# Optimization experiments

Hardware: AMD Instinct MI355X
Metric: run time of the kernel (lower is better)

## Reference

```python
import jax, jax.numpy as jnp
import numpy as np
from jax import lax

NUM_MASKS = 100
NUM_CLASSES = 81  # 80 + 1
KERNEL_DIM = 256
BIAS_PRIOR = float(-np.log((1 - 0.01) / 0.01))


def setup_inputs() -> dict:
    key = jax.random.key(0)
    ks = jax.random.split(key, 12)
    B, C, H, W = 4, 256, 160, 160
    D = C  # expand_dim = in_channels * num_groups
    inp = {
        "features": jax.random.normal(ks[0], (B, C, H, W), jnp.float32),
        # iam_conv: Conv2d(C, num_masks, 3, padding=1)
        "w_iam": jax.random.normal(ks[1], (NUM_MASKS, C, 3, 3), jnp.float32) * 0.01,
        "b_iam": jnp.full((NUM_MASKS,), BIAS_PRIOR, jnp.float32),
        "softmax_bias": jnp.ones((1,), jnp.float32),
        # fc: Linear(D, D), xavier-ish
        "w_fc": jax.random.normal(ks[2], (D, D), jnp.float32) * (1.0 / np.sqrt(D)),
        "b_fc": jnp.zeros((D,), jnp.float32),
        "w_cls": jax.random.normal(ks[3], (NUM_CLASSES, D), jnp.float32) * 0.01,
        "b_cls": jnp.full((NUM_CLASSES,), BIAS_PRIOR, jnp.float32),
        "w_ker": jax.random.normal(ks[4], (KERNEL_DIM, D), jnp.float32) * 0.01,
        "b_ker": jnp.zeros((KERNEL_DIM,), jnp.float32),
        "w_obj": jax.random.normal(ks[5], (1, D), jnp.float32) * (1.0 / np.sqrt(D)),
        "b_obj": jnp.zeros((1,), jnp.float32),
        "w_box": jax.random.normal(ks[6], (4, D), jnp.float32) * 0.01,
        "b_box": jnp.zeros((4,), jnp.float32),
    }
    return inp


def reference(features, w_iam, b_iam, softmax_bias, w_fc, b_fc,
              w_cls, b_cls, w_ker, b_ker, w_obj, b_obj, w_box, b_box):
    B, C, H, W = features.shape
    # conv score map: (B, num_masks, H, W)
    iam = lax.conv_general_dilated(
        features, w_iam, window_strides=(1, 1), padding="SAME",
        dimension_numbers=("NCHW", "OIHW", "NCHW")) + b_iam[None, :, None, None]
    # num_groups == 1: single group iam
    iam_flat = iam.reshape(B, NUM_MASKS, H * W)
    # softmax over HW with learned scalar bias (bias shifts uniformly -> no-op math-wise but kept faithful)
    iam_prob = jax.nn.softmax(iam_flat + softmax_bias[0], axis=-1)  # (B, M, HW)
    # spatial attention pooling: bmm(prob, feats^T) -> (B, M, C)
    inst = jnp.einsum("bmp,bcp->bmc", iam_prob, features.reshape(B, C, H * W))
    # prev_inst_features is None -> skip fc_fuse
    inst = jax.nn.relu(inst @ w_fc.T + b_fc)
    pred_logits = inst @ w_cls.T + b_cls
    pred_kernel = inst @ w_ker.T + b_ker
    pred_scores = inst @ w_obj.T + b_obj
    pred_bboxes = inst @ w_box.T + b_box
    return (pred_logits, pred_kernel, pred_scores, pred_bboxes, iam, inst)
```

## Files before the change

kernel.cpp:

```cpp
#include <hip/hip_runtime.h>
#include <hip/hip_bf16.h>

typedef __attribute__((ext_vector_type(8))) short bf16x8;
typedef __attribute__((ext_vector_type(4))) float f32x4;

#define HW_ 25600
#define HP_ 162
#define WP_ 162

__device__ __forceinline__ unsigned short f2bf(float f) {
    union { float f; unsigned u; } x; x.f = f;
    unsigned r = x.u + 0x7FFFu + ((x.u >> 16) & 1u);
    return (unsigned short)(r >> 16);
}

typedef const __attribute__((address_space(1))) unsigned int* gas_t;
typedef __attribute__((address_space(3))) unsigned int* las_t;
__device__ __forceinline__ void gl_lds16(const void* g, void* l) {
    __builtin_amdgcn_global_load_lds((gas_t)g, (las_t)l, 16, 0, 0);
}

__global__ __launch_bounds__(256) void k_prep(const float* __restrict__ w_iam,
                                              unsigned short* __restrict__ wp,
                                              unsigned short* __restrict__ fpad) {
    int bid = blockIdx.x;
    if (bid < 1152) {
        int idx = bid * 256 + threadIdx.x;
        int stage = idx >> 12;
        int r = idx & 4095;
        int m = r >> 5, cl = r & 31;
        int tap = stage >> 3, kc = stage & 7;
        int jj = (cl >> 3) ^ ((m >> 1) & 3);
        int c = kc * 32 + jj * 8 + (cl & 7);
        int dy = (tap * 11) >> 5, dx = tap - dy * 3;
        float v = (m < 100) ? w_iam[((m * 256 + c) * 3 + dy) * 3 + dx] : 0.f;
        wp[idx] = f2bf(v);
    } else {
        int idx = (bid - 1152) * 256 + threadIdx.x;
        const int perb = 164864;
        if (idx >= 4 * perb) return;
        int b = idx / perb;
        int r = idx - b * perb;
        int hp, wpp, c;
        if (r < 82944) {
            hp = (r < 41472) ? 0 : 161;
            int r2 = r % 41472;
            wpp = r2 >> 8; c = r2 & 255;
        } else {
            r -= 82944;
            wpp = (r < 40960) ? 0 : 161;
            int r2 = r % 40960;
            hp = 1 + (r2 >> 8); c = r2 & 255;
        }
        fpad[((b * HP_ + hp) * WP_ + wpp) * 256 + c] = 0;
    }
}

__global__ __launch_bounds__(256) void k_convert(const float* __restrict__ feat,
                                                 unsigned short* __restrict__ fpad) {
    int bid = blockIdx.x;
    int b = bid / 640;
    int h = (bid >> 2) % 160;
    int c0 = (bid & 3) * 64;
    __shared__ float tile[64][161];
    int t = threadIdx.x;
    const float4* src4 = (const float4*)(feat + ((long)(b * 256 + c0) * 160 + h) * 160);
    #pragma unroll
    for (int s = 0; s < 10; ++s) {
        int q = t + s * 256;
        int ci = q / 40;
        int w4 = q - ci * 40;
        float4 v = src4[(long)ci * 6400 + w4];
        tile[ci][w4 * 4 + 0] = v.x;
        tile[ci][w4 * 4 + 1] = v.y;
        tile[ci][w4 * 4 + 2] = v.z;
        tile[ci][w4 * 4 + 3] = v.w;
    }
    __syncthreads();
    int co = (t & 7) * 8, wq = t >> 3;
    unsigned short* dst = fpad + ((long)(b * HP_ + h + 1) * WP_ + 1) * 256 + c0 + co;
    #pragma unroll
    for (int wp = 0; wp < 5; ++wp) {
        int w = wq + wp * 32;
        bf16x8 v;
        #pragma unroll
        for (int j = 0; j < 8; ++j) v[j] = (short)f2bf(tile[co + j][w]);
        *(bf16x8*)(dst + (long)w * 256) = v;
    }
}

__global__ __launch_bounds__(256, 2) void k_conv(const unsigned short* __restrict__ fpad,
                                                 const unsigned short* __restrict__ wprep,
                                                 const float* __restrict__ b_iam,
                                                 float* __restrict__ iam) {
    int bid = blockIdx.x;
    bid = (bid & 7) * 100 + (bid >> 3);
    int b = bid / 200;
    int p0 = (bid % 200) * 128;
    int tid = threadIdx.x;
    int lane = tid & 63, wid = tid >> 6;
    int wr = wid >> 1, wc = wid & 1;

    __shared__ __align__(16) char smem[2][33024];

    int h0 = p0 / 160, w0 = p0 - h0 * 160;
    int istar = 160 - w0;
    const unsigned short* fb = fpad + (long)b * HP_ * WP_ * 256;

    long rterm[2];
    {
        int c = tid & 3;
        #pragma unroll
        for (int i = 0; i < 2; ++i) {
            int r = i * 64 + (tid >> 2);
            rterm[i] = (long)r * 256 + ((c ^ ((r >> 1) & 3)) << 3);
        }
    }
    long rterm2;
    {
        int r = 128 + ((lane & 15) >> 2), c = lane & 3;
        rterm2 = (long)r * 256 + ((c ^ ((r >> 1) & 3)) << 3);
    }

    f32x4 acc[4][4];
    #pragma unroll
    for (int i = 0; i < 4; ++i)
        #pragma unroll
        for (int j = 0; j < 4; ++j)
            #pragma unroll
            for (int k = 0; k < 4; ++k) acc[i][j][k] = 0.f;

    int aBase = (wr << 12) + ((lane & 15) << 6) + ((((lane >> 4) ^ ((lane >> 1) & 3))) << 4);
    int rb[4];
    #pragma unroll
    for (int nf = 0; nf < 4; ++nf) {
        int i = wc * 64 + nf * 16 + (lane & 15);
        rb[nf] = i + 2 * (i >= istar);
    }

    auto issue = [&](int s, int bi) {
        int dy = s >> 3, kc = s & 7;
        char* Ad = smem[bi];
        char* Bd = smem[bi] + 24576;
        #pragma unroll
        for (int dx = 0; dx < 3; ++dx) {
            const unsigned short* ga = wprep + ((long)((dy * 3 + dx) * 8 + kc) << 12) + (tid << 3);
            char* Adst = Ad + (dx << 13) + (wid << 10);
            gl_lds16(ga, Adst);
            gl_lds16(ga + 2048, Adst + 4096);
        }
        long base = ((long)((h0 + dy) * WP_ + w0)) * 256 + (kc << 5);
        gl_lds16(fb + base + rterm[0], Bd + (wid << 10));
        gl_lds16(fb + base + rterm[1], Bd + 4096 + (wid << 10));
        if (lane < 16) gl_lds16(fb + base + rterm2, Bd + 8192);
    };

    auto compute = [&](int bi) {
        const char* Ab = smem[bi];
        const char* Bb = smem[bi] + 24576;
        #pragma unroll
        for (int dx = 0; dx < 3; ++dx) {
            bf16x8 af[4], bfv[4];
            #pragma unroll
            for (int mf = 0; mf < 4; ++mf)
                af[mf] = *(const bf16x8*)(Ab + (dx << 13) + aBase + (mf << 10));
            #pragma unroll
            for (int nf = 0; nf < 4; ++nf) {
                int row = rb[nf] + dx;
                bfv[nf] = *(const bf16x8*)(Bb + (row << 6) +
                            ((((lane >> 4) ^ ((row >> 1) & 3))) << 4));
            }
            __builtin_amdgcn_s_setprio(1);
            #pragma unroll
            for (int mf = 0; mf < 4; ++mf)
                #pragma unroll
                for (int nf = 0; nf < 4; ++nf)
                    acc[mf][nf] = __builtin_amdgcn_mfma_f32_16x16x32_bf16(
                        af[mf], bfv[nf], acc[mf][nf], 0, 0, 0);
            __builtin_amdgcn_s_setprio(0);
        }
    };

    issue(0, 0);
    for (int s = 0; s < 23; ++s) {
        issue(s + 1, (s + 1) & 1);
        asm volatile("s_waitcnt vmcnt(9)" ::: "memory");
        __builtin_amdgcn_sched_barrier(0);
        __builtin_amdgcn_s_barrier();
        __builtin_amdgcn_sched_barrier(0);
        compute(s & 1);
        __builtin_amdgcn_sched_barrier(0);
        __builtin_amdgcn_s_barrier();
        __builtin_amdgcn_sched_barrier(0);
    }
    asm volatile("s_waitcnt vmcnt(0)" ::: "memory");
    __builtin_amdgcn_sched_barrier(0);
    __builtin_amdgcn_s_barrier();
    __builtin_amdgcn_sched_barrier(0);
    compute(1);

    float* dst = iam + (long)b * 100 * HW_;
    #pragma unroll
    for (int mf = 0; mf < 4; ++mf)
        #pragma unroll
        for (int nf = 0; nf < 4; ++nf) {
            int p = p0 + wc * 64 + nf * 16 + (lane & 15);
            int m0 = wr * 64 + mf * 16 + ((lane >> 4) << 2);
            #pragma unroll
            for (int j = 0; j < 4; ++j) {
                int m = m0 + j;
                if (m < 100) dst[(long)m * HW_ + p] = acc[mf][nf][j] + b_iam[m];
            }
        }
}

__global__ __launch_bounds__(256, 2) void k_pool(const float* __restrict__ feat,
                                                 const float* __restrict__ iam,
                                                 float* __restrict__ partials,
                                                 float* __restrict__ psum) {
    int bid = blockIdx.x;
    int b = bid / 50;
    int slice = bid - b * 50;
    int p0 = slice * 512;
    int tid = threadIdx.x, lane = tid & 63, wq = tid >> 6;

    __shared__ __align__(16) unsigned short A[128 * 72];
    __shared__ __align__(16) unsigned short Bl[256 * 72];
    __shared__ float sums[128];
    if (tid < 128) sums[tid] = 0.f;
    __syncthreads();

    f32x4 acc[7][4];
    #pragma unroll
    for (int i = 0; i < 7; ++i)
        #pragma unroll
        for (int j = 0; j < 4; ++j)
            #pragma unroll
            for (int k = 0; k < 4; ++k) acc[i][j][k] = 0.f;

    int kgrp = (lane >> 4) << 3;

    for (int ks = 0; ks < 8; ++ks) {
        int k0 = p0 + ks * 64;
        for (int s = 0; s < 4; ++s) {
            int q = tid + s * 256;
            int mi = q >> 3, j0 = (q & 7) * 8;
            bf16x8 o;
            if (mi < 100) {
                const float4* sp4 = (const float4*)(iam + (long)(b * 100 + mi) * HW_ + k0 + j0);
                float4 v0 = sp4[0], v1 = sp4[1];
                float xv[8] = {v0.x, v0.y, v0.z, v0.w, v1.x, v1.y, v1.z, v1.w};
                float ls = 0.f;
                #pragma unroll
                for (int j = 0; j < 8; ++j) {
                    float e = __expf(xv[j]);
                    o[j] = (short)f2bf(e);
                    ls += e;
                }
                atomicAdd(&sums[mi], ls);
            } else {
                #pragma unroll
                for (int j = 0; j < 8; ++j) o[j] = 0;
            }
            *(bf16x8*)(A + mi * 72 + j0) = o;
        }
        for (int s = 0; s < 8; ++s) {
            int q = tid + s * 256;
            int ci = q >> 3, j0 = (q & 7) * 8;
            const float4* sp4 = (const float4*)(feat + (long)(b * 256 + ci) * HW_ + k0 + j0);
            float4 v0 = sp4[0], v1 = sp4[1];
            float xv[8] = {v0.x, v0.y, v0.z, v0.w, v1.x, v1.y, v1.z, v1.w};
            bf16x8 o;
            #pragma unroll
            for (int j = 0; j < 8; ++j) o[j] = (short)f2bf(xv[j]);
            *(bf16x8*)(Bl + ci * 72 + j0) = o;
        }
        __syncthreads();
        #pragma unroll
        for (int kk = 0; kk < 64; kk += 32) {
            bf16x8 af[7], bfv[4];
            #pragma unroll
            for (int mf = 0; mf < 7; ++mf)
                af[mf] = *(const bf16x8*)(A + (mf * 16 + (lane & 15)) * 72 + kk + kgrp);
            #pragma unroll
            for (int nf = 0; nf < 4; ++nf)
                bfv[nf] = *(const bf16x8*)(Bl + (wq * 64 + nf * 16 + (lane & 15)) * 72 + kk + kgrp);
            #pragma unroll
            for (int mf = 0; mf < 7; ++mf)
                #pragma unroll
                for (int nf = 0; nf < 4; ++nf)
                    acc[mf][nf] = __builtin_amdgcn_mfma_f32_16x16x32_bf16(
                        af[mf], bfv[nf], acc[mf][nf], 0, 0, 0);
        }
        __syncthreads();
    }
    if (tid < 100) psum[(long)bid * 112 + tid] = sums[tid];
    float* dst = partials + (long)bid * 112 * 256;
    #pragma unroll
    for (int mf = 0; mf < 7; ++mf)
        #pragma unroll
        for (int nf = 0; nf < 4; ++nf) {
            int m0 = mf * 16 + ((lane >> 4) << 2);
            int c  = wq * 64 + nf * 16 + (lane & 15);
            #pragma unroll
            for (int j = 0; j < 4; ++j)
                dst[(long)(m0 + j) * 256 + c] = acc[mf][nf][j];
        }
}

__global__ __launch_bounds__(256) void k_redpool(const float* __restrict__ partials,
                                                 const float* __restrict__ psum,
                                                 float* __restrict__ inst_pool) {
    int bid = blockIdx.x;
    int b = bid / 100, m = bid - b * 100;
    int c = threadIdx.x;
    float s = 0.f, d = 0.f;
    for (int sl = 0; sl < 50; ++sl) {
        s += partials[((long)(b * 50 + sl) * 112 + m) * 256 + c];
        d += psum[(long)(b * 50 + sl) * 112 + m];
    }
    inst_pool[(long)bid * 256 + c] = s / d;
}

__global__ __launch_bounds__(256) void k_fc(const float* __restrict__ inst_pool,
                                            const float* __restrict__ w_fc, const float* __restrict__ b_fc,
                                            const float* __restrict__ w_cls, const float* __restrict__ b_cls,
                                            const float* __restrict__ w_ker, const float* __restrict__ b_ker,
                                            const float* __restrict__ w_obj, const float* __restrict__ b_obj,
                                            const float* __restrict__ w_box, const float* __restrict__ b_box,
                                            float* __restrict__ out) {
    int r = blockIdx.x;
    int t = threadIdx.x;
    __shared__ float row[256];
    __shared__ float inst_s[256];
    row[t] = inst_pool[(long)r * 256 + t];
    __syncthreads();
    {
        float acc = b_fc[t];
        const float4* wv = (const float4*)(w_fc + (long)t * 256);
        for (int c = 0; c < 64; ++c) {
            float4 w4 = wv[c];
            acc += w4.x * row[c * 4] + w4.y * row[c * 4 + 1] + w4.z * row[c * 4 + 2] + w4.w * row[c * 4 + 3];
        }
        acc = fmaxf(acc, 0.f);
        inst_s[t] = acc;
        out[10376800 + (long)r * 256 + t] = acc;
    }
    __syncthreads();
    {
        float acc = b_ker[t];
        const float4* wv = (const float4*)(w_ker + (long)t * 256);
        for (int c = 0; c < 64; ++c) {
            float4 w4 = wv[c];
            acc += w4.x * inst_s[c * 4] + w4.y * inst_s[c * 4 + 1] + w4.z * inst_s[c * 4 + 2] + w4.w * inst_s[c * 4 + 3];
        }
        out[32400 + (long)r * 256 + t] = acc;
    }
    if (t < 81) {
        float acc = b_cls[t];
        const float4* wv = (const float4*)(w_cls + (long)t * 256);
        for (int c = 0; c < 64; ++c) {
            float4 w4 = wv[c];
            acc += w4.x * inst_s[c * 4] + w4.y * inst_s[c * 4 + 1] + w4.z * inst_s[c * 4 + 2] + w4.w * inst_s[c * 4 + 3];
        }
        out[(long)r * 81 + t] = acc;
    }
    if (t == 0) {
        float acc = b_obj[0];
        for (int c = 0; c < 256; ++c) acc += w_obj[c] * inst_s[c];
        out[134800 + r] = acc;
    }
    if (t >= 1 && t < 5) {
        int j = t - 1;
        float acc = b_box[j];
        for (int c = 0; c < 256; ++c) acc += w_box[j * 256 + c] * inst_s[c];
        out[135200 + (long)r * 4 + j] = acc;
    }
}

extern "C" void kernel_launch(void* const* d_in, const int* in_sizes, int n_in,
                              void* d_out, int out_size, void* d_ws, size_t ws_size,
                              hipStream_t stream) {
    const float* feat  = (const float*)d_in[0];
    const float* w_iam = (const float*)d_in[1];
    const float* b_iam = (const float*)d_in[2];
    const float* w_fc  = (const float*)d_in[4];
    const float* b_fc  = (const float*)d_in[5];
    const float* w_cls = (const float*)d_in[6];
    const float* b_cls = (const float*)d_in[7];
    const float* w_ker = (const float*)d_in[8];
    const float* b_ker = (const float*)d_in[9];
    const float* w_obj = (const float*)d_in[10];
    const float* b_obj = (const float*)d_in[11];
    const float* w_box = (const float*)d_in[12];
    const float* b_box = (const float*)d_in[13];
    float* out = (float*)d_out;

    char* ws = (char*)d_ws;
    unsigned short* fpad  = (unsigned short*)ws;
    unsigned short* wprep = (unsigned short*)(ws + 53747712);
    float* partials  = (float*)ws;
    float* psum      = (float*)(ws + 22937600);
    float* inst_pool = (float*)(ws + 23027200);

    float* iam = out + 136800;

    k_prep   <<<dim3(3728), dim3(256), 0, stream>>>(w_iam, wprep, fpad);
    k_convert<<<dim3(2560), dim3(256), 0, stream>>>(feat, fpad);
    k_conv   <<<dim3(800),  dim3(256), 0, stream>>>(fpad, wprep, b_iam, iam);
    k_pool   <<<dim3(200),  dim3(256), 0, stream>>>(feat, iam, partials, psum);
    k_redpool<<<dim3(400),  dim3(256), 0, stream>>>(partials, psum, inst_pool);
    k_fc     <<<dim3(400),  dim3(256), 0, stream>>>(inst_pool, w_fc, b_fc, w_cls, b_cls,
                                                    w_ker, b_ker, w_obj, b_obj, w_box, b_box, out);
}
```

Measured before the change: 191.6 us.

## Fuse softmax exponent into conv epilogue and pool from bf16 copies

The conv epilogue now computes exp of each score, writes it as bf16 to a padded exp buffer and accumulates per-slice row sums. The feature converter also emits an unpadded bf16 copy of the features. A new pool kernel then runs a pipelined bf16 MFMA GEMM directly on these buffers, and the partial reduction and all FC heads are merged into one kernel. This removes the fp32 re-read of iam and features and one launch, at the cost of extra bf16 writes and a larger workspace. Without a max subtraction, the unshifted exp could overflow on other inputs, and the path only runs when the workspace is large enough.

```diff
diff --git a/kernel.cpp b/kernel.cpp
--- a/kernel.cpp
+++ b/kernel.cpp
@@ -3,6 +3,7 @@
 
 typedef __attribute__((ext_vector_type(8))) short bf16x8;
 typedef __attribute__((ext_vector_type(4))) float f32x4;
+typedef __attribute__((ext_vector_type(4))) short short4v;
 
 #define HW_ 25600
 #define HP_ 162
@@ -57,7 +58,8 @@
 }
 
 __global__ __launch_bounds__(256) void k_convert(const float* __restrict__ feat,
-                                                 unsigned short* __restrict__ fpad) {
+                                                 unsigned short* __restrict__ fpad,
+                                                 unsigned short* __restrict__ fcopy) {
     int bid = blockIdx.x;
     int b = bid / 640;
     int h = (bid >> 2) % 160;
@@ -75,6 +77,12 @@
         tile[ci][w4 * 4 + 1] = v.y;
         tile[ci][w4 * 4 + 2] = v.z;
         tile[ci][w4 * 4 + 3] = v.w;
+        if (fcopy) {
+            short4v o;
+            o.x = (short)f2bf(v.x); o.y = (short)f2bf(v.y);
+            o.z = (short)f2bf(v.z); o.w = (short)f2bf(v.w);
+            *(short4v*)(fcopy + ((long)(b * 256 + c0 + ci) * 160 + h) * 160 + w4 * 4) = o;
+        }
     }
     __syncthreads();
     int co = (t & 7) * 8, wq = t >> 3;
@@ -92,11 +100,14 @@
 __global__ __launch_bounds__(256, 2) void k_conv(const unsigned short* __restrict__ fpad,
                                                  const unsigned short* __restrict__ wprep,
                                                  const float* __restrict__ b_iam,
-                                                 float* __restrict__ iam) {
+                                                 float* __restrict__ iam,
+                                                 unsigned short* __restrict__ expiam,
+                                                 float* __restrict__ psum) {
     int bid = blockIdx.x;
     bid = (bid & 7) * 100 + (bid >> 3);
     int b = bid / 200;
-    int p0 = (bid % 200) * 128;
+    int sl = bid % 200;
+    int p0 = sl * 128;
     int tid = threadIdx.x;
     int lane = tid & 63, wid = tid >> 6;
     int wr = wid >> 1, wc = wid & 1;
@@ -199,7 +210,17 @@
     __builtin_amdgcn_sched_barrier(0);
     compute(1);
 
+    bool aux = (expiam != nullptr);
+    __syncthreads();
+    float* sums = (float*)smem[0];
+    if (tid < 128) sums[tid] = 0.f;
+    __syncthreads();
     float* dst = iam + (long)b * 100 * HW_;
+    float sm[4][4];
+    #pragma unroll
+    for (int i = 0; i < 4; ++i)
+        #pragma unroll
+        for (int j = 0; j < 4; ++j) sm[i][j] = 0.f;
     #pragma unroll
     for (int mf = 0; mf < 4; ++mf)
         #pragma unroll
@@ -209,9 +230,207 @@
             #pragma unroll
             for (int j = 0; j < 4; ++j) {
                 int m = m0 + j;
-                if (m < 100) dst[(long)m * HW_ + p] = acc[mf][nf][j] + b_iam[m];
+                if (m < 100) {
+                    float v = acc[mf][nf][j] + b_iam[m];
+                    dst[(long)m * HW_ + p] = v;
+                    if (aux) {
+                        float e = __expf(v);
+                        expiam[((long)(b * 128 + m)) * HW_ + p] = f2bf(e);
+                        sm[mf][j] += e;
+                    }
+                } else if (aux) {
+                    expiam[((long)(b * 128 + m)) * HW_ + p] = 0;
+                }
             }
         }
+    if (aux) {
+        #pragma unroll
+        for (int mf = 0; mf < 4; ++mf)
+            #pragma unroll
+            for (int j = 0; j < 4; ++j) {
+                float r = sm[mf][j];
+                r += __shfl_xor(r, 1); r += __shfl_xor(r, 2);
+                r += __shfl_xor(r, 4); r += __shfl_xor(r, 8);
+                if ((lane & 15) == 0) {
+                    int m = wr * 64 + mf * 16 + ((lane >> 4) << 2) + j;
+                    if (m < 100) atomicAdd(&sums[m], r);
+                }
+            }
+        __syncthreads();
+        if (tid < 100) psum[((long)b * 200 + sl) * 128 + tid] = sums[tid];
+    }
+}
+
+__global__ __launch_bounds__(256, 1) void k_poolf(const unsigned short* __restrict__ expiam,
+                                                  const unsigned short* __restrict__ fcopy,
+                                                  float* __restrict__ partials) {
+    int bid = blockIdx.x;
+    int b = bid / 50;
+    int slice = bid - b * 50;
+    int p0 = slice * 512;
+    int tid = threadIdx.x, lane = tid & 63, wid = tid >> 6;
+
+    __shared__ __align__(16) char smem[2][49152];
+
+    f32x4 acc[8][4];
+    #pragma unroll
+    for (int i = 0; i < 8; ++i)
+        #pragma unroll
+        for (int j = 0; j < 4; ++j)
+            #pragma unroll
+            for (int k = 0; k < 4; ++k) acc[i][j][k] = 0.f;
+
+    const unsigned short* eb = expiam + (long)b * 128 * HW_;
+    const unsigned short* fb = fcopy + (long)b * 256 * HW_;
+
+    auto issue = [&](int ks, int bi) {
+        int k0 = p0 + ks * 64;
+        char* Ad = smem[bi];
+        char* Bd = smem[bi] + 16384;
+        #pragma unroll
+        for (int s = 0; s < 4; ++s) {
+            int slot = tid + s * 256;
+            int mi = slot >> 3, ch = slot & 7;
+            gl_lds16(eb + (long)mi * HW_ + k0 + ((ch ^ (mi & 7)) << 3),
+                     Ad + (s << 12) + (wid << 10));
+        }
+        #pragma unroll
+        for (int s = 0; s < 8; ++s) {
+            int slot = tid + s * 256;
+            int cj = slot >> 3, ch = slot & 7;
+            gl_lds16(fb + (long)cj * HW_ + k0 + ((ch ^ (cj & 7)) << 3),
+                     Bd + (s << 12) + (wid << 10));
+        }
+    };
+
+    auto compute = [&](int bi) {
+        const char* Ab = smem[bi];
+        const char* Bb = smem[bi] + 16384;
+        #pragma unroll
+        for (int kk = 0; kk < 2; ++kk) {
+            bf16x8 af[8], bfv[4];
+            #pragma unroll
+            for (int mf = 0; mf < 8; ++mf) {
+                int m = mf * 16 + (lane & 15);
+                int c = (kk << 2) + (lane >> 4);
+                af[mf] = *(const bf16x8*)(Ab + (m << 7) + (((c ^ (m & 7))) << 4));
+            }
+            #pragma unroll
+            for (int nf = 0; nf < 4; ++nf) {
+                int cr = wid * 64 + nf * 16 + (lane & 15);
+                int c = (kk << 2) + (lane >> 4);
+                bfv[nf] = *(const bf16x8*)(Bb + (cr << 7) + (((c ^ (cr & 7))) << 4));
+            }
+            __builtin_amdgcn_s_setprio(1);
+            #pragma unroll
+            for (int mf = 0; mf < 8; ++mf)
+                #pragma unroll
+                for (int nf = 0; nf < 4; ++nf)
+                    acc[mf][nf] = __builtin_amdgcn_mfma_f32_16x16x32_bf16(
+                        af[mf], bfv[nf], acc[mf][nf], 0, 0, 0);
+            __builtin_amdgcn_s_setprio(0);
+        }
+    };
+
+    issue(0, 0);
+    for (int s = 0; s < 8; ++s) {
+        if (s < 7) {
+            issue(s + 1, (s + 1) & 1);
+            asm volatile("s_waitcnt vmcnt(12)" ::: "memory");
+        } else {
+            asm volatile("s_waitcnt vmcnt(0)" ::: "memory");
+        }
+        __builtin_amdgcn_sched_barrier(0);
+        __builtin_amdgcn_s_barrier();
+        __builtin_amdgcn_sched_barrier(0);
+        compute(s & 1);
+        __builtin_amdgcn_sched_barrier(0);
+        __builtin_amdgcn_s_barrier();
+        __builtin_amdgcn_sched_barrier(0);
+    }
+
+    float* dst = partials + (long)bid * 128 * 256;
+    #pragma unroll
+    for (int mf = 0; mf < 8; ++mf)
+        #pragma unroll
+        for (int nf = 0; nf < 4; ++nf) {
+            int m0 = mf * 16 + ((lane >> 4) << 2);
+            int c  = wid * 64 + nf * 16 + (lane & 15);
+            #pragma unroll
+            for (int j = 0; j < 4; ++j)
+                dst[(long)(m0 + j) * 256 + c] = acc[mf][nf][j];
+        }
+}
+
+__global__ __launch_bounds__(256) void k_redfc(const float* __restrict__ partials,
+                                               const float* __restrict__ psum,
+                                               const float* __restrict__ w_fc, const float* __restrict__ b_fc,
+                                               const float* __restrict__ w_cls, const float* __restrict__ b_cls,
+                                               const float* __restrict__ w_ker, const float* __restrict__ b_ker,
+                                               const float* __restrict__ w_obj, const float* __restrict__ b_obj,
+                                               const float* __restrict__ w_box, const float* __restrict__ b_box,
+                                               float* __restrict__ out) {
+    int r = blockIdx.x;
+    int b = r / 100, m = r - b * 100;
+    int t = threadIdx.x;
+    __shared__ float red[256];
+    __shared__ float row[256];
+    __shared__ float inst_s[256];
+
+    red[t] = (t < 200) ? psum[((long)b * 200 + t) * 128 + m] : 0.f;
+    __syncthreads();
+    for (int o = 128; o > 0; o >>= 1) {
+        if (t < o) red[t] += red[t + o];
+        __syncthreads();
+    }
+    float d = red[0];
+
+    float s = 0.f;
+    for (int sl = 0; sl < 50; ++sl)
+        s += partials[((long)(b * 50 + sl) * 128 + m) * 256 + t];
+    row[t] = s / d;
+    __syncthreads();
+    {
+        float acc = b_fc[t];
+        const float4* wv = (const float4*)(w_fc + (long)t * 256);
+        for (int c = 0; c < 64; ++c) {
+            float4 w4 = wv[c];
+            acc += w4.x * row[c * 4] + w4.y * row[c * 4 + 1] + w4.z * row[c * 4 + 2] + w4.w * row[c * 4 + 3];
+        }
+        acc = fmaxf(acc, 0.f);
+        inst_s[t] = acc;
+        out[10376800 + (long)r * 256 + t] = acc;
+    }
+    __syncthreads();
+    {
+        float acc = b_ker[t];
+        const float4* wv = (const float4*)(w_ker + (long)t * 256);
+        for (int c = 0; c < 64; ++c) {
+            float4 w4 = wv[c];
+            acc += w4.x * inst_s[c * 4] + w4.y * inst_s[c * 4 + 1] + w4.z * inst_s[c * 4 + 2] + w4.w * inst_s[c * 4 + 3];
+        }
+        out[32400 + (long)r * 256 + t] = acc;
+    }
+    if (t < 81) {
+        float acc = b_cls[t];
+        const float4* wv = (const float4*)(w_cls + (long)t * 256);
+        for (int c = 0; c < 64; ++c) {
+            float4 w4 = wv[c];
+            acc += w4.x * inst_s[c * 4] + w4.y * inst_s[c * 4 + 1] + w4.z * inst_s[c * 4 + 2] + w4.w * inst_s[c * 4 + 3];
+        }
+        out[(long)r * 81 + t] = acc;
+    }
+    if (t == 0) {
+        float acc = b_obj[0];
+        for (int c = 0; c < 256; ++c) acc += w_obj[c] * inst_s[c];
+        out[134800 + r] = acc;
+    }
+    if (t >= 1 && t < 5) {
+        int j = t - 1;
+        float acc = b_box[j];
+        for (int c = 0; c < 256; ++c) acc += w_box[j * 256 + c] * inst_s[c];
+        out[135200 + (long)r * 4 + j] = acc;
+    }
 }
 
 __global__ __launch_bounds__(256, 2) void k_pool(const float* __restrict__ feat,
@@ -399,17 +618,34 @@
     char* ws = (char*)d_ws;
     unsigned short* fpad  = (unsigned short*)ws;
     unsigned short* wprep = (unsigned short*)(ws + 53747712);
-    float* partials  = (float*)ws;
-    float* psum      = (float*)(ws + 22937600);
-    float* inst_pool = (float*)(ws + 23027200);
-
     float* iam = out + 136800;
 
-    k_prep   <<<dim3(3728), dim3(256), 0, stream>>>(w_iam, wprep, fpad);
-    k_convert<<<dim3(2560), dim3(256), 0, stream>>>(feat, fpad);
-    k_conv   <<<dim3(800),  dim3(256), 0, stream>>>(fpad, wprep, b_iam, iam);
-    k_pool   <<<dim3(200),  dim3(256), 0, stream>>>(feat, iam, partials, psum);
-    k_redpool<<<dim3(400),  dim3(256), 0, stream>>>(partials, psum, inst_pool);
-    k_fc     <<<dim3(400),  dim3(256), 0, stream>>>(inst_pool, w_fc, b_fc, w_cls, b_cls,
-                                                    w_ker, b_ker, w_obj, b_obj, w_box, b_box, out);
-}
+    const size_t NEED_FAST = 133390336ULL;
+    bool fast = (ws_size >= NEED_FAST);
+
+    k_prep<<<dim3(3728), dim3(256), 0, stream>>>(w_iam, wprep, fpad);
+
+    if (fast) {
+        unsigned short* fcopy  = (unsigned short*)(ws + 54337536);
+        unsigned short* expiam = (unsigned short*)(ws + 106766336);
+        float* psum            = (float*)(ws + 132980736);
+        float* partials        = (float*)ws;
+
+        k_convert<<<dim3(2560), dim3(256), 0, stream>>>(feat, fpad, fcopy);
+        k_conv   <<<dim3(800),  dim3(256), 0, stream>>>(fpad, wprep, b_iam, iam, expiam, psum);
+        k_poolf  <<<dim3(200),  dim3(256), 0, stream>>>(expiam, fcopy, partials);
+        k_redfc  <<<dim3(400),  dim3(256), 0, stream>>>(partials, psum, w_fc, b_fc, w_cls, b_cls,
+                                                        w_ker, b_ker, w_obj, b_obj, w_box, b_box, out);
+    } else {
+        float* partials  = (float*)ws;
+        float* psum      = (float*)(ws + 22937600);
+        float* inst_pool = (float*)(ws + 23027200);
+
+        k_convert<<<dim3(2560), dim3(256), 0, stream>>>(feat, fpad, nullptr);
+        k_conv   <<<dim3(800),  dim3(256), 0, stream>>>(fpad, wprep, b_iam, iam, nullptr, nullptr);
+        k_pool   <<<dim3(200),  dim3(256), 0, stream>>>(feat, iam, partials, psum);
+        k_redpool<<<dim3(400),  dim3(256), 0, stream>>>(partials, psum, inst_pool);
+        k_fc     <<<dim3(400),  dim3(256), 0, stream>>>(inst_pool, w_fc, b_fc, w_cls, b_cls,
+                                                        w_ker, b_ker, w_obj, b_obj, w_box, b_box, out);
+    }
+}
```

Result: slower. 199.4 us (+4.1%).

## Reuse bf16 feature copy in pooling and fuse reduction with FC heads

Applied to the files above, without the earlier changes.

While converting features, k_convert now also writes a bf16 copy in NCHW layout. A new 512-thread pooling kernel streams that copy into swizzled LDS via direct global-to-LDS loads, instead of re-reading and converting the fp32 features. The partial-sum reduction and the FC heads are merged into one kernel, which removes a launch and the inst_pool round trip. The fast path only runs when the workspace is large enough; the extra bf16 write adds traffic during conversion.

```diff
diff --git a/kernel.cpp b/kernel.cpp
--- a/kernel.cpp
+++ b/kernel.cpp
@@ -3,6 +3,7 @@
 
 typedef __attribute__((ext_vector_type(8))) short bf16x8;
 typedef __attribute__((ext_vector_type(4))) float f32x4;
+typedef __attribute__((ext_vector_type(4))) short short4v;
 
 #define HW_ 25600
 #define HP_ 162
@@ -57,7 +58,8 @@
 }
 
 __global__ __launch_bounds__(256) void k_convert(const float* __restrict__ feat,
-                                                 unsigned short* __restrict__ fpad) {
+                                                 unsigned short* __restrict__ fpad,
+                                                 unsigned short* __restrict__ fcopy) {
     int bid = blockIdx.x;
     int b = bid / 640;
     int h = (bid >> 2) % 160;
@@ -75,6 +77,12 @@
         tile[ci][w4 * 4 + 1] = v.y;
         tile[ci][w4 * 4 + 2] = v.z;
         tile[ci][w4 * 4 + 3] = v.w;
+        if (fcopy) {
+            short4v o;
+            o.x = (short)f2bf(v.x); o.y = (short)f2bf(v.y);
+            o.z = (short)f2bf(v.z); o.w = (short)f2bf(v.w);
+            *(short4v*)(fcopy + ((long)(b * 256 + c0 + ci) * 160 + h) * 160 + w4 * 4) = o;
+        }
     }
     __syncthreads();
     int co = (t & 7) * 8, wq = t >> 3;
@@ -214,6 +222,179 @@
         }
 }
 
+__global__ __launch_bounds__(512, 4) void k_pool2(const float* __restrict__ iam,
+                                                  const unsigned short* __restrict__ fcopy,
+                                                  float* __restrict__ partials,
+                                                  float* __restrict__ psum) {
+    int bid = blockIdx.x;
+    int b = bid / 50;
+    int slice = bid - b * 50;
+    int p0 = slice * 512;
+    int tid = threadIdx.x, lane = tid & 63, wid = tid >> 6;
+    int wrr = wid >> 2, wcc = wid & 3;
+
+    __shared__ __align__(16) unsigned short A[128 * 72];
+    __shared__ __align__(16) unsigned short Bl[256 * 64];
+    __shared__ float sums[128];
+    if (tid < 128) sums[tid] = 0.f;
+
+    f32x4 acc[4][4];
+    #pragma unroll
+    for (int i = 0; i < 4; ++i)
+        #pragma unroll
+        for (int j = 0; j < 4; ++j)
+            #pragma unroll
+            for (int k = 0; k < 4; ++k) acc[i][j][k] = 0.f;
+
+    const unsigned short* fb = fcopy + (long)b * 256 * HW_;
+    const float* ib = iam + (long)b * 100 * HW_;
+    int kgrp = (lane >> 4) << 3;
+
+    __syncthreads();
+
+    for (int ks = 0; ks < 8; ++ks) {
+        int k0 = p0 + ks * 64;
+        #pragma unroll
+        for (int s = 0; s < 4; ++s) {
+            int slot = tid + s * 512;
+            int cj = slot >> 3, ch = slot & 7;
+            gl_lds16(fb + (long)cj * HW_ + k0 + ((ch ^ (cj & 7)) << 3),
+                     (char*)Bl + (s << 13) + (wid << 10));
+        }
+        #pragma unroll
+        for (int s = 0; s < 2; ++s) {
+            int q = tid + s * 512;
+            int mi = q >> 3, j0 = (q & 7) * 8;
+            bf16x8 o;
+            if (mi < 100) {
+                const float4* sp4 = (const float4*)(ib + (long)mi * HW_ + k0 + j0);
+                float4 v0 = sp4[0], v1 = sp4[1];
+                float xv[8] = {v0.x, v0.y, v0.z, v0.w, v1.x, v1.y, v1.z, v1.w};
+                float ls = 0.f;
+                #pragma unroll
+                for (int j = 0; j < 8; ++j) {
+                    float e = __expf(xv[j]);
+                    o[j] = (short)f2bf(e);
+                    ls += e;
+                }
+                atomicAdd(&sums[mi], ls);
+            } else {
+                #pragma unroll
+                for (int j = 0; j < 8; ++j) o[j] = 0;
+            }
+            *(bf16x8*)(A + mi * 72 + j0) = o;
+        }
+        __syncthreads();
+        #pragma unroll
+        for (int kk = 0; kk < 64; kk += 32) {
+            bf16x8 af[4], bfv[4];
+            #pragma unroll
+            for (int mf = 0; mf < 4; ++mf)
+                af[mf] = *(const bf16x8*)(A + (wrr * 64 + mf * 16 + (lane & 15)) * 72 + kk + kgrp);
+            #pragma unroll
+            for (int nf = 0; nf < 4; ++nf) {
+                int cr = wcc * 64 + nf * 16 + (lane & 15);
+                int c = (kk >> 3) + (lane >> 4);
+                bfv[nf] = *(const bf16x8*)((const char*)Bl + (cr << 7) + ((c ^ (cr & 7)) << 4));
+            }
+            __builtin_amdgcn_s_setprio(1);
+            #pragma unroll
+            for (int mf = 0; mf < 4; ++mf)
+                #pragma unroll
+                for (int nf = 0; nf < 4; ++nf)
+                    acc[mf][nf] = __builtin_amdgcn_mfma_f32_16x16x32_bf16(
+                        af[mf], bfv[nf], acc[mf][nf], 0, 0, 0);
+            __builtin_amdgcn_s_setprio(0);
+        }
+        __syncthreads();
+    }
+    if (tid < 100) psum[(long)bid * 112 + tid] = sums[tid];
+    float* dst = partials + (long)bid * 112 * 256;
+    #pragma unroll
+    for (int mf = 0; mf < 4; ++mf)
+        #pragma unroll
+        for (int nf = 0; nf < 4; ++nf) {
+            int m0 = wrr * 64 + mf * 16 + ((lane >> 4) << 2);
+            int c  = wcc * 64 + nf * 16 + (lane & 15);
+            #pragma unroll
+            for (int j = 0; j < 4; ++j) {
+                int m = m0 + j;
+                if (m < 112) dst[(long)m * 256 + c] = acc[mf][nf][j];
+            }
+        }
+}
+
+__global__ __launch_bounds__(256) void k_redfc(const float* __restrict__ partials,
+                                               const float* __restrict__ psum,
+                                               const float* __restrict__ w_fc, const float* __restrict__ b_fc,
+                                               const float* __restrict__ w_cls, const float* __restrict__ b_cls,
+                                               const float* __restrict__ w_ker, const float* __restrict__ b_ker,
+                                               const float* __restrict__ w_obj, const float* __restrict__ b_obj,
+                                               const float* __restrict__ w_box, const float* __restrict__ b_box,
+                                               float* __restrict__ out) {
+    int r = blockIdx.x;
+    int b = r / 100, m = r - b * 100;
+    int t = threadIdx.x;
+    __shared__ float red[256];
+    __shared__ float row[256];
+    __shared__ float inst_s[256];
+
+    red[t] = (t < 50) ? psum[(long)(b * 50 + t) * 112 + m] : 0.f;
+    __syncthreads();
+    for (int o = 128; o > 0; o >>= 1) {
+        if (t < o) red[t] += red[t + o];
+        __syncthreads();
+    }
+    float d = red[0];
+
+    float s = 0.f;
+    for (int sl = 0; sl < 50; ++sl)
+        s += partials[((long)(b * 50 + sl) * 112 + m) * 256 + t];
+    row[t] = s / d;
+    __syncthreads();
+    {
+        float acc = b_fc[t];
+        const float4* wv = (const float4*)(w_fc + (long)t * 256);
+        for (int c = 0; c < 64; ++c) {
+            float4 w4 = wv[c];
+            acc += w4.x * row[c * 4] + w4.y * row[c * 4 + 1] + w4.z * row[c * 4 + 2] + w4.w * row[c * 4 + 3];
+        }
+        acc = fmaxf(acc, 0.f);
+        inst_s[t] = acc;
+        out[10376800 + (long)r * 256 + t] = acc;
+    }
+    __syncthreads();
+    {
+        float acc = b_ker[t];
+        const float4* wv = (const float4*)(w_ker + (long)t * 256);
+        for (int c = 0; c < 64; ++c) {
+            float4 w4 = wv[c];
+            acc += w4.x * inst_s[c * 4] + w4.y * inst_s[c * 4 + 1] + w4.z * inst_s[c * 4 + 2] + w4.w * inst_s[c * 4 + 3];
+        }
+        out[32400 + (long)r * 256 + t] = acc;
+    }
+    if (t < 81) {
+        float acc = b_cls[t];
+        const float4* wv = (const float4*)(w_cls + (long)t * 256);
+        for (int c = 0; c < 64; ++c) {
+            float4 w4 = wv[c];
+            acc += w4.x * inst_s[c * 4] + w4.y * inst_s[c * 4 + 1] + w4.z * inst_s[c * 4 + 2] + w4.w * inst_s[c * 4 + 3];
+        }
+        out[(long)r * 81 + t] = acc;
+    }
+    if (t == 0) {
+        float acc = b_obj[0];
+        for (int c = 0; c < 256; ++c) acc += w_obj[c] * inst_s[c];
+        out[134800 + r] = acc;
+    }
+    if (t >= 1 && t < 5) {
+        int j = t - 1;
+        float acc = b_box[j];
+        for (int c = 0; c < 256; ++c) acc += w_box[j * 256 + c] * inst_s[c];
+        out[135200 + (long)r * 4 + j] = acc;
+    }
+}
+
 __global__ __launch_bounds__(256, 2) void k_pool(const float* __restrict__ feat,
                                                  const float* __restrict__ iam,
                                                  float* __restrict__ partials,
@@ -306,76 +487,6 @@
             for (int j = 0; j < 4; ++j)
                 dst[(long)(m0 + j) * 256 + c] = acc[mf][nf][j];
         }
-}
-
-__global__ __launch_bounds__(256) void k_redpool(const float* __restrict__ partials,
-                                                 const float* __restrict__ psum,
-                                                 float* __restrict__ inst_pool) {
-    int bid = blockIdx.x;
-    int b = bid / 100, m = bid - b * 100;
-    int c = threadIdx.x;
-    float s = 0.f, d = 0.f;
-    for (int sl = 0; sl < 50; ++sl) {
-        s += partials[((long)(b * 50 + sl) * 112 + m) * 256 + c];
-        d += psum[(long)(b * 50 + sl) * 112 + m];
-    }
-    inst_pool[(long)bid * 256 + c] = s / d;
-}
-
-__global__ __launch_bounds__(256) void k_fc(const float* __restrict__ inst_pool,
-                                            const float* __restrict__ w_fc, const float* __restrict__ b_fc,
-                                            const float* __restrict__ w_cls, const float* __restrict__ b_cls,
-                                            const float* __restrict__ w_ker, const float* __restrict__ b_ker,
-                                            const float* __restrict__ w_obj, const float* __restrict__ b_obj,
-                                            const float* __restrict__ w_box, const float* __restrict__ b_box,
-                                            float* __restrict__ out) {
-    int r = blockIdx.x;
-    int t = threadIdx.x;
-    __shared__ float row[256];
-    __shared__ float inst_s[256];
-    row[t] = inst_pool[(long)r * 256 + t];
-    __syncthreads();
-    {
-        float acc = b_fc[t];
-        const float4* wv = (const float4*)(w_fc + (long)t * 256);
-        for (int c = 0; c < 64; ++c) {
-            float4 w4 = wv[c];
-            acc += w4.x * row[c * 4] + w4.y * row[c * 4 + 1] + w4.z * row[c * 4 + 2] + w4.w * row[c * 4 + 3];
-        }
-        acc = fmaxf(acc, 0.f);
-        inst_s[t] = acc;
-        out[10376800 + (long)r * 256 + t] = acc;
-    }
-    __syncthreads();
-    {
-        float acc = b_ker[t];
-        const float4* wv = (const float4*)(w_ker + (long)t * 256);
-        for (int c = 0; c < 64; ++c) {
-            float4 w4 = wv[c];
-            acc += w4.x * inst_s[c * 4] + w4.y * inst_s[c * 4 + 1] + w4.z * inst_s[c * 4 + 2] + w4.w * inst_s[c * 4 + 3];
-        }
-        out[32400 + (long)r * 256 + t] = acc;
-    }
-    if (t < 81) {
-        float acc = b_cls[t];
-        const float4* wv = (const float4*)(w_cls + (long)t * 256);
-        for (int c = 0; c < 64; ++c) {
-            float4 w4 = wv[c];
-            acc += w4.x * inst_s[c * 4] + w4.y * inst_s[c * 4 + 1] + w4.z * inst_s[c * 4 + 2] + w4.w * inst_s[c * 4 + 3];
-        }
-        out[(long)r * 81 + t] = acc;
-    }
-    if (t == 0) {
-        float acc = b_obj[0];
-        for (int c = 0; c < 256; ++c) acc += w_obj[c] * inst_s[c];
-        out[134800 + r] = acc;
-    }
-    if (t >= 1 && t < 5) {
-        int j = t - 1;
-        float acc = b_box[j];
-        for (int c = 0; c < 256; ++c) acc += w_box[j * 256 + c] * inst_s[c];
-        out[135200 + (long)r * 4 + j] = acc;
-    }
 }
 
 extern "C" void kernel_launch(void* const* d_in, const int* in_sizes, int n_in,
@@ -399,17 +510,26 @@
     char* ws = (char*)d_ws;
     unsigned short* fpad  = (unsigned short*)ws;
     unsigned short* wprep = (unsigned short*)(ws + 53747712);
-    float* partials  = (float*)ws;
-    float* psum      = (float*)(ws + 22937600);
-    float* inst_pool = (float*)(ws + 23027200);
-
     float* iam = out + 136800;
 
-    k_prep   <<<dim3(3728), dim3(256), 0, stream>>>(w_iam, wprep, fpad);
-    k_convert<<<dim3(2560), dim3(256), 0, stream>>>(feat, fpad);
-    k_conv   <<<dim3(800),  dim3(256), 0, stream>>>(fpad, wprep, b_iam, iam);
-    k_pool   <<<dim3(200),  dim3(256), 0, stream>>>(feat, iam, partials, psum);
-    k_redpool<<<dim3(400),  dim3(256), 0, stream>>>(partials, psum, inst_pool);
-    k_fc     <<<dim3(400),  dim3(256), 0, stream>>>(inst_pool, w_fc, b_fc, w_cls, b_cls,
-                                                    w_ker, b_ker, w_obj, b_obj, w_box, b_box, out);
-}
+    float* partials = (float*)ws;
+    float* psum     = (float*)(ws + 22937600);
+
+    const size_t NEED_FAST = 106766336ULL;
+    bool fast = (ws_size >= NEED_FAST);
+
+    k_prep<<<dim3(3728), dim3(256), 0, stream>>>(w_iam, wprep, fpad);
+
+    if (fast) {
+        unsigned short* fcopy = (unsigned short*)(ws + 54337536);
+        k_convert<<<dim3(2560), dim3(256), 0, stream>>>(feat, fpad, fcopy);
+        k_conv   <<<dim3(800),  dim3(256), 0, stream>>>(fpad, wprep, b_iam, iam);
+        k_pool2  <<<dim3(200),  dim3(512), 0, stream>>>(iam, fcopy, partials, psum);
+    } else {
+        k_convert<<<dim3(2560), dim3(256), 0, stream>>>(feat, fpad, nullptr);
+        k_conv   <<<dim3(800),  dim3(256), 0, stream>>>(fpad, wprep, b_iam, iam);
+        k_pool   <<<dim3(200),  dim3(256), 0, stream>>>(feat, iam, partials, psum);
+    }
+    k_redfc<<<dim3(400), dim3(256), 0, stream>>>(partials, psum, w_fc, b_fc, w_cls, b_cls,
+                                                 w_ker, b_ker, w_obj, b_obj, w_box, b_box, out);
+}
```

Result: slower. 200.5 us (+4.6%).

## Single-buffer conv weight tiles to fit three blocks per CU, fuse reduce into FC

Applied to the files above, without the earlier changes.

The conv kernel now keeps only one LDS buffer for the weight (A) tiles and double-buffers just the feature (B) tiles. This cuts LDS per block from about 66KB to about 41KB, and launch bounds are raised to allow three blocks per CU. The A load for the next step is now issued after compute, so its latency is exposed before the next barrier rather than overlapped with compute. Separately, the partial-sum reduction is fused into the FC kernel, which removes one launch and the intermediate buffer round trip.

```diff
diff --git a/kernel.cpp b/kernel.cpp
--- a/kernel.cpp
+++ b/kernel.cpp
@@ -89,7 +89,7 @@
     }
 }
 
-__global__ __launch_bounds__(256, 2) void k_conv(const unsigned short* __restrict__ fpad,
+__global__ __launch_bounds__(256, 3) void k_conv(const unsigned short* __restrict__ fpad,
                                                  const unsigned short* __restrict__ wprep,
                                                  const float* __restrict__ b_iam,
                                                  float* __restrict__ iam) {
@@ -101,7 +101,7 @@
     int lane = tid & 63, wid = tid >> 6;
     int wr = wid >> 1, wc = wid & 1;
 
-    __shared__ __align__(16) char smem[2][33024];
+    __shared__ __align__(16) char smem[24576 + 2 * 8448];
 
     int h0 = p0 / 160, w0 = p0 - h0 * 160;
     int istar = 160 - w0;
@@ -138,17 +138,19 @@
         rb[nf] = i + 2 * (i >= istar);
     }
 
-    auto issue = [&](int s, int bi) {
+    auto issueA = [&](int s) {
         int dy = s >> 3, kc = s & 7;
-        char* Ad = smem[bi];
-        char* Bd = smem[bi] + 24576;
         #pragma unroll
         for (int dx = 0; dx < 3; ++dx) {
             const unsigned short* ga = wprep + ((long)((dy * 3 + dx) * 8 + kc) << 12) + (tid << 3);
-            char* Adst = Ad + (dx << 13) + (wid << 10);
+            char* Adst = smem + (dx << 13) + (wid << 10);
             gl_lds16(ga, Adst);
             gl_lds16(ga + 2048, Adst + 4096);
         }
+    };
+    auto issueB = [&](int s, int bi) {
+        int dy = s >> 3, kc = s & 7;
+        char* Bd = smem + 24576 + bi * 8448;
         long base = ((long)((h0 + dy) * WP_ + w0)) * 256 + (kc << 5);
         gl_lds16(fb + base + rterm[0], Bd + (wid << 10));
         gl_lds16(fb + base + rterm[1], Bd + 4096 + (wid << 10));
@@ -156,8 +158,8 @@
     };
 
     auto compute = [&](int bi) {
-        const char* Ab = smem[bi];
-        const char* Bb = smem[bi] + 24576;
+        const char* Ab = smem;
+        const char* Bb = smem + 24576 + bi * 8448;
         #pragma unroll
         for (int dx = 0; dx < 3; ++dx) {
             bf16x8 af[4], bfv[4];
@@ -181,10 +183,15 @@
         }
     };
 
-    issue(0, 0);
-    for (int s = 0; s < 23; ++s) {
-        issue(s + 1, (s + 1) & 1);
-        asm volatile("s_waitcnt vmcnt(9)" ::: "memory");
+    issueB(0, 0);
+    issueA(0);
+    for (int s = 0; s < 24; ++s) {
+        if (s < 23) {
+            issueB(s + 1, (s + 1) & 1);
+            asm volatile("s_waitcnt vmcnt(3)" ::: "memory");
+        } else {
+            asm volatile("s_waitcnt vmcnt(0)" ::: "memory");
+        }
         __builtin_amdgcn_sched_barrier(0);
         __builtin_amdgcn_s_barrier();
         __builtin_amdgcn_sched_barrier(0);
@@ -192,12 +199,8 @@
         __builtin_amdgcn_sched_barrier(0);
         __builtin_amdgcn_s_barrier();
         __builtin_amdgcn_sched_barrier(0);
-    }
-    asm volatile("s_waitcnt vmcnt(0)" ::: "memory");
-    __builtin_amdgcn_sched_barrier(0);
-    __builtin_amdgcn_s_barrier();
-    __builtin_amdgcn_sched_barrier(0);
-    compute(1);
+        if (s < 23) issueA(s + 1);
+    }
 
     float* dst = iam + (long)b * 100 * HW_;
     #pragma unroll
@@ -308,32 +311,33 @@
         }
 }
 
-__global__ __launch_bounds__(256) void k_redpool(const float* __restrict__ partials,
-                                                 const float* __restrict__ psum,
-                                                 float* __restrict__ inst_pool) {
-    int bid = blockIdx.x;
-    int b = bid / 100, m = bid - b * 100;
-    int c = threadIdx.x;
-    float s = 0.f, d = 0.f;
-    for (int sl = 0; sl < 50; ++sl) {
-        s += partials[((long)(b * 50 + sl) * 112 + m) * 256 + c];
-        d += psum[(long)(b * 50 + sl) * 112 + m];
-    }
-    inst_pool[(long)bid * 256 + c] = s / d;
-}
-
-__global__ __launch_bounds__(256) void k_fc(const float* __restrict__ inst_pool,
-                                            const float* __restrict__ w_fc, const float* __restrict__ b_fc,
-                                            const float* __restrict__ w_cls, const float* __restrict__ b_cls,
-                                            const float* __restrict__ w_ker, const float* __restrict__ b_ker,
-                                            const float* __restrict__ w_obj, const float* __restrict__ b_obj,
-                                            const float* __restrict__ w_box, const float* __restrict__ b_box,
-                                            float* __restrict__ out) {
+__global__ __launch_bounds__(256) void k_redfc(const float* __restrict__ partials,
+                                               const float* __restrict__ psum,
+                                               const float* __restrict__ w_fc, const float* __restrict__ b_fc,
+                                               const float* __restrict__ w_cls, const float* __restrict__ b_cls,
+                                               const float* __restrict__ w_ker, const float* __restrict__ b_ker,
+                                               const float* __restrict__ w_obj, const float* __restrict__ b_obj,
+                                               const float* __restrict__ w_box, const float* __restrict__ b_box,
+                                               float* __restrict__ out) {
     int r = blockIdx.x;
+    int b = r / 100, m = r - b * 100;
     int t = threadIdx.x;
+    __shared__ float red[256];
     __shared__ float row[256];
     __shared__ float inst_s[256];
-    row[t] = inst_pool[(long)r * 256 + t];
+
+    red[t] = (t < 50) ? psum[(long)(b * 50 + t) * 112 + m] : 0.f;
+    __syncthreads();
+    for (int o = 128; o > 0; o >>= 1) {
+        if (t < o) red[t] += red[t + o];
+        __syncthreads();
+    }
+    float d = red[0];
+
+    float s = 0.f;
+    for (int sl = 0; sl < 50; ++sl)
+        s += partials[((long)(b * 50 + sl) * 112 + m) * 256 + t];
+    row[t] = s / d;
     __syncthreads();
     {
         float acc = b_fc[t];
@@ -399,17 +403,15 @@
     char* ws = (char*)d_ws;
     unsigned short* fpad  = (unsigned short*)ws;
     unsigned short* wprep = (unsigned short*)(ws + 53747712);
-    float* partials  = (float*)ws;
-    float* psum      = (float*)(ws + 22937600);
-    float* inst_pool = (float*)(ws + 23027200);
-
     float* iam = out + 136800;
+
+    float* partials = (float*)ws;
+    float* psum     = (float*)(ws + 22937600);
 
     k_prep   <<<dim3(3728), dim3(256), 0, stream>>>(w_iam, wprep, fpad);
     k_convert<<<dim3(2560), dim3(256), 0, stream>>>(feat, fpad);
     k_conv   <<<dim3(800),  dim3(256), 0, stream>>>(fpad, wprep, b_iam, iam);
     k_pool   <<<dim3(200),  dim3(256), 0, stream>>>(feat, iam, partials, psum);
-    k_redpool<<<dim3(400),  dim3(256), 0, stream>>>(partials, psum, inst_pool);
-    k_fc     <<<dim3(400),  dim3(256), 0, stream>>>(inst_pool, w_fc, b_fc, w_cls, b_cls,
+    k_redfc  <<<dim3(400),  dim3(256), 0, stream>>>(partials, psum, w_fc, b_fc, w_cls, b_cls,
                                                     w_ker, b_ker, w_obj, b_obj, w_box, b_box, out);
 }
```

After: 195.1 us. Within noise of the previous version (+1.8%).
